# Optimization experiments

Measured on AMD Instinct MI355X. Metric: run time of the kernel, lower is better.

The kernel has to match this reference:

```python
import jax, jax.numpy as jnp
import numpy as np

B, C_IN, C_OUT, H, W = 32, 256, 256, 56, 56
RATE = 0.5
K = int(C_OUT * (1.0 - RATE))  # 128 channels zeroed
BN_EPS = 1e-5


def setup_inputs() -> dict:
    key = jax.random.key(0)
    ks = jax.random.split(key, 4)
    return {
        "x": jax.random.normal(ks[0], (B, C_IN, H, W), dtype=jnp.float32),
        "conv_w": jax.random.normal(ks[1], (C_OUT, C_IN, 3, 3), dtype=jnp.float32) * 0.05,
        "gate_w": jax.random.normal(ks[2], (C_OUT, C_IN), dtype=jnp.float32) * 0.05,
        "gate_b": jnp.ones((C_OUT,), dtype=jnp.float32),
        "bn_gamma": jnp.ones((C_OUT,), dtype=jnp.float32),
        "bn_beta": jnp.zeros((C_OUT,), dtype=jnp.float32),
        "bn_mean": jnp.zeros((C_OUT,), dtype=jnp.float32),
        "bn_var": jnp.ones((C_OUT,), dtype=jnp.float32),
    }


def reference(x, conv_w, gate_w, gate_b, bn_gamma, bn_beta, bn_mean, bn_var):
    # conv2: 3x3, stride 1, padding 1, no bias  -> [B, C_OUT, H, W]
    y = jax.lax.conv_general_dilated(
        x, conv_w, window_strides=(1, 1), padding=((1, 1), (1, 1)),
        dimension_numbers=("NCHW", "OIHW", "NCHW"))
    # BatchNorm2d (eval mode: running stats)
    inv = bn_gamma / jnp.sqrt(bn_var + BN_EPS)
    y = y * inv[None, :, None, None] + (bn_beta - bn_mean * inv)[None, :, None, None]
    # use_relu=True
    y = jax.nn.relu(y)
    # gate: global abs-avg-pool -> linear -> relu   [B, C_OUT]
    s = jnp.mean(jnp.abs(x), axis=(2, 3))  # [B, C_IN]
    g = jax.nn.relu(s @ gate_w.T + gate_b)
    # zero the K smallest gate values per row (topk of -g), then renormalize
    _, idx = jax.lax.top_k(-g, K)  # indices of K smallest
    t = g.at[jnp.arange(B)[:, None], idx].set(0.0)
    t = t / jnp.sum(t, axis=1, keepdims=True) * C_OUT
    # broadcast channel mask
    return y * t[:, :, None, None]
```

## Files before the change

### kernel.cpp

```cpp
#include <hip/hip_runtime.h>
#include <hip/hip_bf16.h>
#include <cstdint>

typedef unsigned short ushort_t;
typedef unsigned int uint_t;
typedef __bf16 bf16x8 __attribute__((ext_vector_type(8)));
typedef float f32x4 __attribute__((ext_vector_type(4)));

#define B_SZ 32
#define C_IN 256
#define C_OUT 256
#define H_SZ 56
#define W_SZ 56
#define HW 3136
#define HP 58
#define WP 58
#define BN_EPS 1e-5f
#define K_ZERO 128

__device__ __forceinline__ ushort_t f2bf(float f) {
    unsigned int u = __builtin_bit_cast(unsigned int, f);
    unsigned int r = (u + 0x7fffu + ((u >> 16) & 1u)) >> 16;
    return (ushort_t)r;
}

__device__ __forceinline__ void load_lds16(const void* gptr, void* ldsptr) {
    __builtin_amdgcn_global_load_lds(
        (const __attribute__((address_space(1))) unsigned int*)(uintptr_t)gptr,
        (__attribute__((address_space(3))) unsigned int*)(uintptr_t)ldsptr,
        16, 0, 0);
}

__global__ __launch_bounds__(256) void prep_x_kernel(const float* __restrict__ x,
                                                     ushort_t* __restrict__ xbp,
                                                     float* __restrict__ s) {
    const int cit = blockIdx.x, h = blockIdx.y, b = blockIdx.z;
    __shared__ float tile[64][57];
    __shared__ float red2[256];
    const int t = threadIdx.x;
    const float* src = x + ((size_t)(b * C_IN + cit * 64) * H_SZ + h) * W_SZ;
    for (int i = t; i < 64 * 14; i += 256) {
        int ci = i / 14, w4 = (i - ci * 14) * 4;
        float4 v = *(const float4*)(src + (size_t)ci * HW + w4);
        tile[ci][w4] = v.x; tile[ci][w4 + 1] = v.y;
        tile[ci][w4 + 2] = v.z; tile[ci][w4 + 3] = v.w;
    }
    __syncthreads();
    {
        int ci = t & 63, wg = t >> 6;
        float a = 0.f;
#pragma unroll
        for (int j = 0; j < 14; j++) a += fabsf(tile[ci][wg * 14 + j]);
        red2[t] = a;
    }
    __syncthreads();
    if (t < 64) {
        float tot = red2[t] + red2[t + 64] + red2[t + 128] + red2[t + 192];
        atomicAdd(&s[b * C_IN + cit * 64 + t], tot * (1.0f / (float)HW));
    }
    for (int i = t; i < W_SZ * 16; i += 256) {
        int w = i >> 4, c4 = (i & 15) * 4;
        uint_t lo = (uint_t)f2bf(tile[c4][w])     | ((uint_t)f2bf(tile[c4 + 1][w]) << 16);
        uint_t hi = (uint_t)f2bf(tile[c4 + 2][w]) | ((uint_t)f2bf(tile[c4 + 3][w]) << 16);
        size_t dst = ((size_t)((b * HP + h + 1) * WP + (w + 1))) * C_IN + cit * 64 + c4;
        *(uint2*)&xbp[dst] = make_uint2(lo, hi);
    }
}

__global__ __launch_bounds__(256) void prep_w_kernel(const float* __restrict__ w,
                                                     const float* __restrict__ gamma,
                                                     const float* __restrict__ beta,
                                                     const float* __restrict__ mean,
                                                     const float* __restrict__ var,
                                                     ushort_t* __restrict__ Wt,
                                                     float* __restrict__ bninv,
                                                     float* __restrict__ bnadd) {
    int idx = blockIdx.x * 256 + threadIdx.x;
    if (idx < 9 * C_OUT * C_IN) {
        int tap = idx >> 16;
        int rem = idx & 65535;
        int co = rem >> 8, ci = rem & 255;
        Wt[idx] = f2bf(w[(size_t)(co * C_IN + ci) * 9 + tap]);
    }
    if (blockIdx.x == 0 && threadIdx.x < C_OUT) {
        int c = threadIdx.x;
        float inv = gamma[c] * rsqrtf(var[c] + BN_EPS);
        bninv[c] = inv;
        bnadd[c] = beta[c] - mean[c] * inv;
    }
}

__global__ __launch_bounds__(256) void gate_kernel(const float* __restrict__ s,
                                                   const float* __restrict__ gw,
                                                   const float* __restrict__ gb,
                                                   float* __restrict__ tscale) {
    const int b = blockIdx.x, t = threadIdx.x;
    __shared__ float sh_s[C_IN], sh_g[C_OUT], red[256];
    sh_s[t] = s[b * C_IN + t];
    __syncthreads();
    float acc = gb[t];
    const float* wr = gw + (size_t)t * C_IN;
    for (int ci = 0; ci < C_IN; ci++) acc += sh_s[ci] * wr[ci];
    float g = fmaxf(acc, 0.f);
    sh_g[t] = g;
    __syncthreads();
    int cnt = 0;
    for (int j = 0; j < C_OUT; j++) {
        float gj = sh_g[j];
        cnt += (gj < g) || (gj == g && j < t);
    }
    float tv = (cnt >= K_ZERO) ? g : 0.f;
    red[t] = tv;
    __syncthreads();
    for (int off = 128; off > 0; off >>= 1) {
        if (t < off) red[t] += red[t + off];
        __syncthreads();
    }
    tscale[b * C_OUT + t] = tv * ((float)C_OUT / red[0]);
}

__global__ __launch_bounds__(256) void conv_kernel(const ushort_t* __restrict__ xbp,
                                                   const ushort_t* __restrict__ Wt,
                                                   const float* __restrict__ bninv,
                                                   const float* __restrict__ bnadd,
                                                   const float* __restrict__ tscale,
                                                   float* __restrict__ out) {
    __shared__ __align__(16) ushort_t As[128 * 64];
    __shared__ __align__(16) ushort_t Bs[128 * 64];
    const int t = threadIdx.x;
    const int bx = blockIdx.x;
    const int by = blockIdx.y;
    const int lane = t & 63;
    const int wv = t >> 6;
    const int waveM = wv >> 1, waveN = wv & 1;

    const int srow = t >> 3;
    const int gxor8 = ((t & 7) ^ (srow & 7)) * 8;
    int arow[4], wrow[4];
#pragma unroll
    for (int i = 0; i < 4; i++) {
        int p = bx * 128 + i * 32 + srow;
        int b = p / HW;
        int r = p - b * HW;
        int hh = r / W_SZ, ww = r - hh * W_SZ;
        arow[i] = ((b * HP + hh + 1) * WP + (ww + 1)) * C_IN + gxor8;
        wrow[i] = (by * 128 + i * 32 + srow) * C_IN + gxor8;
    }
    ushort_t* ldsA = As + t * 8;
    ushort_t* ldsB = Bs + t * 8;

    int aoff[2][4], boff[2][4];
#pragma unroll
    for (int ks = 0; ks < 2; ks++)
#pragma unroll
        for (int mt = 0; mt < 4; mt++) {
            int c = (lane >> 4) + ks * 4;
            int ra = waveM * 64 + mt * 16 + (lane & 15);
            aoff[ks][mt] = (ra * 8 + (c ^ (ra & 7))) * 16;
            int rb = waveN * 64 + mt * 16 + (lane & 15);
            boff[ks][mt] = (rb * 8 + (c ^ (rb & 7))) * 16;
        }

    f32x4 acc[4][4];
#pragma unroll
    for (int i = 0; i < 4; i++)
#pragma unroll
        for (int j = 0; j < 4; j++) acc[i][j] = (f32x4){0.f, 0.f, 0.f, 0.f};

    const char* Ab = (const char*)As;
    const char* Bb = (const char*)Bs;

    for (int tap = 0; tap < 9; tap++) {
        const int doff = ((tap / 3 - 1) * WP + (tap % 3 - 1)) * C_IN;
        const int woff = tap * (C_OUT * C_IN);
#pragma unroll
        for (int cq = 0; cq < 4; cq++) {
            const int ci0 = cq * 64;
#pragma unroll
            for (int i = 0; i < 4; i++) {
                load_lds16(xbp + arow[i] + doff + ci0, ldsA + i * 2048);
                load_lds16(Wt + wrow[i] + woff + ci0, ldsB + i * 2048);
            }
            __syncthreads();
#pragma unroll
            for (int ks = 0; ks < 2; ks++) {
                bf16x8 af[4], bf[4];
#pragma unroll
                for (int mt = 0; mt < 4; mt++) af[mt] = *(const bf16x8*)(Ab + aoff[ks][mt]);
#pragma unroll
                for (int nt = 0; nt < 4; nt++) bf[nt] = *(const bf16x8*)(Bb + boff[ks][nt]);
#pragma unroll
                for (int mt = 0; mt < 4; mt++)
#pragma unroll
                    for (int nt = 0; nt < 4; nt++)
                        acc[mt][nt] = __builtin_amdgcn_mfma_f32_16x16x32_bf16(
                            af[mt], bf[nt], acc[mt][nt], 0, 0, 0);
            }
            __syncthreads();
        }
    }

#pragma unroll
    for (int mt = 0; mt < 4; mt++) {
        int p0 = bx * 128 + waveM * 64 + mt * 16 + (lane >> 4) * 4;
        int b = p0 / HW;
        int hw = p0 - b * HW;
#pragma unroll
        for (int nt = 0; nt < 4; nt++) {
            int co = by * 128 + waveN * 64 + nt * 16 + (lane & 15);
            float inv = bninv[co], add = bnadd[co], tsc = tscale[b * C_OUT + co];
            float4 o;
            o.x = fmaxf(acc[mt][nt][0] * inv + add, 0.f) * tsc;
            o.y = fmaxf(acc[mt][nt][1] * inv + add, 0.f) * tsc;
            o.z = fmaxf(acc[mt][nt][2] * inv + add, 0.f) * tsc;
            o.w = fmaxf(acc[mt][nt][3] * inv + add, 0.f) * tsc;
            *(float4*)(out + (size_t)(b * C_OUT + co) * HW + hw) = o;
        }
    }
}

extern "C" void kernel_launch(void* const* d_in, const int* in_sizes, int n_in,
                              void* d_out, int out_size, void* d_ws, size_t ws_size,
                              hipStream_t stream) {
    const float* x      = (const float*)d_in[0];
    const float* conv_w = (const float*)d_in[1];
    const float* gate_w = (const float*)d_in[2];
    const float* gate_b = (const float*)d_in[3];
    const float* bn_g   = (const float*)d_in[4];
    const float* bn_b   = (const float*)d_in[5];
    const float* bn_m   = (const float*)d_in[6];
    const float* bn_v   = (const float*)d_in[7];
    float* out = (float*)d_out;

    char* ws = (char*)d_ws;
    float*    s      = (float*)(ws + 0);
    float*    tscale = (float*)(ws + 32768);
    float*    bninv  = (float*)(ws + 65536);
    float*    bnadd  = (float*)(ws + 66560);
    ushort_t* Wt     = (ushort_t*)(ws + 67584);
    ushort_t* xbp    = (ushort_t*)(ws + 1247232);

    hipMemsetAsync(s, 0, 32768, stream);
    hipMemsetAsync(xbp, 0, (size_t)B_SZ * HP * WP * C_IN * 2, stream);
    prep_x_kernel<<<dim3(4, 56, 32), 256, 0, stream>>>(x, xbp, s);
    prep_w_kernel<<<2304, 256, 0, stream>>>(conv_w, bn_g, bn_b, bn_m, bn_v, Wt, bninv, bnadd);
    gate_kernel<<<32, 256, 0, stream>>>(s, gate_w, gate_b, tscale);
    conv_kernel<<<dim3(784, 2), 256, 0, stream>>>(xbp, Wt, bninv, bnadd, tscale, out);
}
```

Baseline: 385.2 us.

## Widen conv tile to all output channels and drop memsets via in-kernel zeroing

The conv kernel now computes all 256 output channels per block (128x256 tile, 4x8 MFMA tiles per wave). Each block loads its activation tile once instead of twice across two blocks. The padded-input memset is replaced by writing only the halo borders inside prep_x, and the gate-sum memset is folded into prep_w, which now runs first. In exchange, accumulator registers double (128 floats per thread) and LDS grows, which risks lower occupancy or spilling despite launch_bounds(256,2).

Result: slower. 405.8 us (+5.3%).

```diff
diff --git a/kernel.cpp b/kernel.cpp
--- a/kernel.cpp
+++ b/kernel.cpp
@@ -29,6 +29,31 @@
         (const __attribute__((address_space(1))) unsigned int*)(uintptr_t)gptr,
         (__attribute__((address_space(3))) unsigned int*)(uintptr_t)ldsptr,
         16, 0, 0);
+}
+
+__global__ __launch_bounds__(256) void prep_w_kernel(const float* __restrict__ w,
+                                                     const float* __restrict__ gamma,
+                                                     const float* __restrict__ beta,
+                                                     const float* __restrict__ mean,
+                                                     const float* __restrict__ var,
+                                                     ushort_t* __restrict__ Wt,
+                                                     float* __restrict__ bninv,
+                                                     float* __restrict__ bnadd,
+                                                     float* __restrict__ s) {
+    int idx = blockIdx.x * 256 + threadIdx.x;
+    if (idx < 9 * C_OUT * C_IN) {
+        int tap = idx >> 16;
+        int rem = idx & 65535;
+        int co = rem >> 8, ci = rem & 255;
+        Wt[idx] = f2bf(w[(size_t)(co * C_IN + ci) * 9 + tap]);
+    }
+    if (blockIdx.x < 32) s[idx] = 0.f;
+    if (blockIdx.x == 32 && threadIdx.x < C_OUT) {
+        int c = threadIdx.x;
+        float inv = gamma[c] * rsqrtf(var[c] + BN_EPS);
+        bninv[c] = inv;
+        bnadd[c] = beta[c] - mean[c] * inv;
+    }
 }
 
 __global__ __launch_bounds__(256) void prep_x_kernel(const float* __restrict__ x,
@@ -58,6 +83,7 @@
         float tot = red2[t] + red2[t + 64] + red2[t + 128] + red2[t + 192];
         atomicAdd(&s[b * C_IN + cit * 64 + t], tot * (1.0f / (float)HW));
     }
+    const uint2 z2 = make_uint2(0u, 0u);
     for (int i = t; i < W_SZ * 16; i += 256) {
         int w = i >> 4, c4 = (i & 15) * 4;
         uint_t lo = (uint_t)f2bf(tile[c4][w])     | ((uint_t)f2bf(tile[c4 + 1][w]) << 16);
@@ -65,28 +91,18 @@
         size_t dst = ((size_t)((b * HP + h + 1) * WP + (w + 1))) * C_IN + cit * 64 + c4;
         *(uint2*)&xbp[dst] = make_uint2(lo, hi);
     }
-}
-
-__global__ __launch_bounds__(256) void prep_w_kernel(const float* __restrict__ w,
-                                                     const float* __restrict__ gamma,
-                                                     const float* __restrict__ beta,
-                                                     const float* __restrict__ mean,
-                                                     const float* __restrict__ var,
-                                                     ushort_t* __restrict__ Wt,
-                                                     float* __restrict__ bninv,
-                                                     float* __restrict__ bnadd) {
-    int idx = blockIdx.x * 256 + threadIdx.x;
-    if (idx < 9 * C_OUT * C_IN) {
-        int tap = idx >> 16;
-        int rem = idx & 65535;
-        int co = rem >> 8, ci = rem & 255;
-        Wt[idx] = f2bf(w[(size_t)(co * C_IN + ci) * 9 + tap]);
-    }
-    if (blockIdx.x == 0 && threadIdx.x < C_OUT) {
-        int c = threadIdx.x;
-        float inv = gamma[c] * rsqrtf(var[c] + BN_EPS);
-        bninv[c] = inv;
-        bnadd[c] = beta[c] - mean[c] * inv;
+    if (t < 32) {
+        int side = t >> 4, c4 = (t & 15) * 4;
+        size_t dst = ((size_t)((b * HP + h + 1) * WP + side * 57)) * C_IN + cit * 64 + c4;
+        *(uint2*)&xbp[dst] = z2;
+    }
+    if (h == 0 || h == 55) {
+        int prow = (h == 0) ? 0 : 57;
+        for (int i = t; i < 58 * 16; i += 256) {
+            int w = i >> 4, c4 = (i & 15) * 4;
+            size_t dst = ((size_t)((b * HP + prow) * WP + w)) * C_IN + cit * 64 + c4;
+            *(uint2*)&xbp[dst] = z2;
+        }
     }
 }
 
@@ -119,24 +135,23 @@
     tscale[b * C_OUT + t] = tv * ((float)C_OUT / red[0]);
 }
 
-__global__ __launch_bounds__(256) void conv_kernel(const ushort_t* __restrict__ xbp,
-                                                   const ushort_t* __restrict__ Wt,
-                                                   const float* __restrict__ bninv,
-                                                   const float* __restrict__ bnadd,
-                                                   const float* __restrict__ tscale,
-                                                   float* __restrict__ out) {
+__global__ __launch_bounds__(256, 2) void conv_kernel(const ushort_t* __restrict__ xbp,
+                                                      const ushort_t* __restrict__ Wt,
+                                                      const float* __restrict__ bninv,
+                                                      const float* __restrict__ bnadd,
+                                                      const float* __restrict__ tscale,
+                                                      float* __restrict__ out) {
     __shared__ __align__(16) ushort_t As[128 * 64];
-    __shared__ __align__(16) ushort_t Bs[128 * 64];
+    __shared__ __align__(16) ushort_t Bs[256 * 64];
     const int t = threadIdx.x;
     const int bx = blockIdx.x;
-    const int by = blockIdx.y;
     const int lane = t & 63;
     const int wv = t >> 6;
     const int waveM = wv >> 1, waveN = wv & 1;
 
     const int srow = t >> 3;
     const int gxor8 = ((t & 7) ^ (srow & 7)) * 8;
-    int arow[4], wrow[4];
+    int arow[4], wrow[8];
 #pragma unroll
     for (int i = 0; i < 4; i++) {
         int p = bx * 128 + i * 32 + srow;
@@ -144,28 +159,33 @@
         int r = p - b * HW;
         int hh = r / W_SZ, ww = r - hh * W_SZ;
         arow[i] = ((b * HP + hh + 1) * WP + (ww + 1)) * C_IN + gxor8;
-        wrow[i] = (by * 128 + i * 32 + srow) * C_IN + gxor8;
-    }
+    }
+#pragma unroll
+    for (int i = 0; i < 8; i++) wrow[i] = (i * 32 + srow) * C_IN + gxor8;
     ushort_t* ldsA = As + t * 8;
     ushort_t* ldsB = Bs + t * 8;
 
-    int aoff[2][4], boff[2][4];
-#pragma unroll
-    for (int ks = 0; ks < 2; ks++)
+    int aoff[2][4], boff[2][8];
+#pragma unroll
+    for (int ks = 0; ks < 2; ks++) {
+        int c = (lane >> 4) + ks * 4;
 #pragma unroll
         for (int mt = 0; mt < 4; mt++) {
-            int c = (lane >> 4) + ks * 4;
             int ra = waveM * 64 + mt * 16 + (lane & 15);
             aoff[ks][mt] = (ra * 8 + (c ^ (ra & 7))) * 16;
-            int rb = waveN * 64 + mt * 16 + (lane & 15);
-            boff[ks][mt] = (rb * 8 + (c ^ (rb & 7))) * 16;
-        }
-
-    f32x4 acc[4][4];
+        }
+#pragma unroll
+        for (int nt = 0; nt < 8; nt++) {
+            int rb = waveN * 128 + nt * 16 + (lane & 15);
+            boff[ks][nt] = (rb * 8 + (c ^ (rb & 7))) * 16;
+        }
+    }
+
+    f32x4 acc[4][8];
 #pragma unroll
     for (int i = 0; i < 4; i++)
 #pragma unroll
-        for (int j = 0; j < 4; j++) acc[i][j] = (f32x4){0.f, 0.f, 0.f, 0.f};
+        for (int j = 0; j < 8; j++) acc[i][j] = (f32x4){0.f, 0.f, 0.f, 0.f};
 
     const char* Ab = (const char*)As;
     const char* Bb = (const char*)Bs;
@@ -177,22 +197,23 @@
         for (int cq = 0; cq < 4; cq++) {
             const int ci0 = cq * 64;
 #pragma unroll
-            for (int i = 0; i < 4; i++) {
+            for (int i = 0; i < 4; i++)
                 load_lds16(xbp + arow[i] + doff + ci0, ldsA + i * 2048);
+#pragma unroll
+            for (int i = 0; i < 8; i++)
                 load_lds16(Wt + wrow[i] + woff + ci0, ldsB + i * 2048);
-            }
             __syncthreads();
 #pragma unroll
             for (int ks = 0; ks < 2; ks++) {
-                bf16x8 af[4], bf[4];
+                bf16x8 af[4], bf[8];
 #pragma unroll
                 for (int mt = 0; mt < 4; mt++) af[mt] = *(const bf16x8*)(Ab + aoff[ks][mt]);
 #pragma unroll
-                for (int nt = 0; nt < 4; nt++) bf[nt] = *(const bf16x8*)(Bb + boff[ks][nt]);
+                for (int nt = 0; nt < 8; nt++) bf[nt] = *(const bf16x8*)(Bb + boff[ks][nt]);
 #pragma unroll
                 for (int mt = 0; mt < 4; mt++)
 #pragma unroll
-                    for (int nt = 0; nt < 4; nt++)
+                    for (int nt = 0; nt < 8; nt++)
                         acc[mt][nt] = __builtin_amdgcn_mfma_f32_16x16x32_bf16(
                             af[mt], bf[nt], acc[mt][nt], 0, 0, 0);
             }
@@ -206,8 +227,8 @@
         int b = p0 / HW;
         int hw = p0 - b * HW;
 #pragma unroll
-        for (int nt = 0; nt < 4; nt++) {
-            int co = by * 128 + waveN * 64 + nt * 16 + (lane & 15);
+        for (int nt = 0; nt < 8; nt++) {
+            int co = waveN * 128 + nt * 16 + (lane & 15);
             float inv = bninv[co], add = bnadd[co], tsc = tscale[b * C_OUT + co];
             float4 o;
             o.x = fmaxf(acc[mt][nt][0] * inv + add, 0.f) * tsc;
@@ -240,10 +261,8 @@
     ushort_t* Wt     = (ushort_t*)(ws + 67584);
     ushort_t* xbp    = (ushort_t*)(ws + 1247232);
 
-    hipMemsetAsync(s, 0, 32768, stream);
-    hipMemsetAsync(xbp, 0, (size_t)B_SZ * HP * WP * C_IN * 2, stream);
+    prep_w_kernel<<<2304, 256, 0, stream>>>(conv_w, bn_g, bn_b, bn_m, bn_v, Wt, bninv, bnadd, s);
     prep_x_kernel<<<dim3(4, 56, 32), 256, 0, stream>>>(x, xbp, s);
-    prep_w_kernel<<<2304, 256, 0, stream>>>(conv_w, bn_g, bn_b, bn_m, bn_v, Wt, bninv, bnadd);
     gate_kernel<<<32, 256, 0, stream>>>(s, gate_w, gate_b, tscale);
-    conv_kernel<<<dim3(784, 2), 256, 0, stream>>>(xbp, Wt, bninv, bnadd, tscale, out);
-}
+    conv_kernel<<<784, 256, 0, stream>>>(xbp, Wt, bninv, bnadd, tscale, out);
+}
```
